# Performance work log

Hardware: AMD Instinct MI355X
Metric: run time of the kernel (lower is better)

The kernel has to match this reference:

```python
import jax, jax.numpy as jnp
import numpy as np

EPS = 1e-5
CONV_THRESHOLD = 0.0


def setup_inputs() -> dict:
    key = jax.random.key(0)
    ks = jax.random.split(key, 16)
    B, F = 65536, 256
    H1, H2 = 1024, 512
    d_in = F + 1  # raw features + 1 scalar conv feature
    inp = {
        "x": jax.random.normal(ks[0], (B, F), dtype=jnp.float32),
        # layer 1: Linear(d_in, H1) + BatchNorm1d(H1)
        "W1": jax.random.normal(ks[1], (d_in, H1), dtype=jnp.float32) * (1.0 / np.sqrt(d_in)),
        "b1": jax.random.normal(ks[2], (H1,), dtype=jnp.float32) * 0.01,
        "g1": jnp.ones((H1,), jnp.float32) + 0.1 * jax.random.normal(ks[3], (H1,), dtype=jnp.float32),
        "be1": jax.random.normal(ks[4], (H1,), dtype=jnp.float32) * 0.01,
        "m1": jax.random.normal(ks[5], (H1,), dtype=jnp.float32) * 0.1,
        "v1": jax.random.uniform(ks[6], (H1,), dtype=jnp.float32, minval=0.5, maxval=1.5),
        # layer 2: Linear(H1, H2) + BatchNorm1d(H2)
        "W2": jax.random.normal(ks[7], (H1, H2), dtype=jnp.float32) * (1.0 / np.sqrt(H1)),
        "b2": jax.random.normal(ks[8], (H2,), dtype=jnp.float32) * 0.01,
        "g2": jnp.ones((H2,), jnp.float32) + 0.1 * jax.random.normal(ks[9], (H2,), dtype=jnp.float32),
        "be2": jax.random.normal(ks[10], (H2,), dtype=jnp.float32) * 0.01,
        "m2": jax.random.normal(ks[11], (H2,), dtype=jnp.float32) * 0.1,
        "v2": jax.random.uniform(ks[12], (H2,), dtype=jnp.float32, minval=0.5, maxval=1.5),
        # output head: Linear(H2, 1)
        "W3": jax.random.normal(ks[13], (H2, 1), dtype=jnp.float32) * (1.0 / np.sqrt(H2)),
        "b3": jax.random.normal(ks[14], (1,), dtype=jnp.float32) * 0.01,
    }
    return inp


def _bn(h, g, be, m, v):
    # eval-mode BatchNorm1d with running statistics
    return g * (h - m) * jax.lax.rsqrt(v + EPS) + be


def reference(x, W1, b1, g1, be1, m1, v1, W2, b2, g2, be2, m2, v2, W3, b3):
    # Batched replacement of the per-sample numpy threshold conv:
    # the Conv filter reduces the whole sample patch with a mean and thresholds it,
    # producing one binary scalar feature per sample.  [B, 1]
    conv_feat = jnp.where(jnp.mean(x, axis=1, keepdims=True) > CONV_THRESHOLD, 1.0, 0.0).astype(x.dtype)
    h = jnp.concatenate([x, conv_feat], axis=1)  # [B, F+1]
    h = jax.nn.relu(_bn(h @ W1 + b1, g1, be1, m1, v1))  # [B, H1]
    h = jax.nn.relu(_bn(h @ W2 + b2, g2, be2, m2, v2))  # [B, H2]
    return jax.nn.sigmoid(h @ W3 + b3)  # [B, 1]
```

## Files before the change

kernel.cpp:

```cpp
#include <hip/hip_runtime.h>
#include <hip/hip_bf16.h>
#include <cstdint>
#include <cstddef>

typedef __bf16 bf16_t;
typedef bf16_t bf16x8 __attribute__((ext_vector_type(8)));
typedef float f32x4 __attribute__((ext_vector_type(4)));

#define BN_EPS 1e-5f

__device__ __forceinline__ void async_load16(const bf16_t* g, bf16_t* lds) {
  __builtin_amdgcn_global_load_lds(
      (__attribute__((address_space(1))) uint32_t*)(g),
      (__attribute__((address_space(3))) uint32_t*)(lds),
      16, 0, 0);
}

__global__ void prep_weights_kernel(const float* __restrict__ W1, const float* __restrict__ W2,
                                    const float* b1, const float* g1, const float* be1,
                                    const float* m1, const float* v1,
                                    const float* b2, const float* g2, const float* be2,
                                    const float* m2, const float* v2,
                                    bf16_t* __restrict__ W1T, bf16_t* __restrict__ W2T,
                                    float* s1, float* t1, float* s2, float* t2,
                                    float* w1last) {
  const int b = blockIdx.x;
  if (b < 192) {
    const float* src;
    bf16_t* dst;
    int R, C, bx, by;
    if (b < 64) { src = W1; dst = W1T; R = 256; C = 1024; bx = b & 15; by = b >> 4; }
    else        { src = W2; dst = W2T; R = 1024; C = 512; bx = (b - 64) & 7; by = (b - 64) >> 3; }
    __shared__ bf16_t tile[64][66];
    const int r0 = by * 64, c0 = bx * 64;
    const int tc = threadIdx.x & 63;
    const int tr4 = threadIdx.x >> 6;
#pragma unroll
    for (int i = 0; i < 16; ++i) {
      int r = i * 4 + tr4;
      tile[r][tc] = (bf16_t)src[(size_t)(r0 + r) * C + c0 + tc];
    }
    __syncthreads();
#pragma unroll
    for (int i = 0; i < 16; ++i) {
      int rr = i * 4 + tr4;
      dst[(size_t)(c0 + rr) * R + r0 + tc] = tile[tc][rr];
    }
  } else {
    for (int i = threadIdx.x; i < 1024; i += 256) {
      float s = g1[i] * rsqrtf(v1[i] + BN_EPS);
      s1[i] = s;
      t1[i] = be1[i] - m1[i] * s + b1[i] * s;
      w1last[i] = W1[256 * 1024 + i];
      if (i < 512) {
        float s2v = g2[i] * rsqrtf(v2[i] + BN_EPS);
        s2[i] = s2v;
        t2[i] = be2[i] - m2[i] * s2v + b2[i] * s2v;
      }
    }
  }
}

__global__ __launch_bounds__(256, 2) void fused_mlp(
    const float* __restrict__ x,
    const bf16_t* __restrict__ W1T, const bf16_t* __restrict__ W2T,
    const float* __restrict__ s1, const float* __restrict__ t1,
    const float* __restrict__ w1last,
    const float* __restrict__ s2, const float* __restrict__ t2,
    const float* __restrict__ W3, const float* __restrict__ b3,
    float* __restrict__ out) {
  __shared__ __align__(16) unsigned char smem[73728];
  const int tid = threadIdx.x;
  const int lane = tid & 63;
  const int w = tid >> 6;
  const int l15 = lane & 15;
  const int quad = lane >> 4;
  const int mTile = blockIdx.x * 64;

  bf16_t* As = (bf16_t*)smem;
  bf16_t* h1c = (bf16_t*)(smem + 32768);
  float* convs = (float*)(smem + 32768);
  bf16_t* B1s = (bf16_t*)(smem + 65536);
  float* outW = (float*)(smem + 65536);

  {
    const int rsub = lane >> 5;
    const int cc = lane & 31;
#pragma unroll
    for (int i = 0; i < 8; ++i) {
      int row = w * 16 + i * 2 + rsub;
      const float* gx = x + (size_t)(mTile + row) * 256 + cc * 8;
      const float4 a = *(const float4*)gx;
      const float4 bq = *(const float4*)(gx + 4);
      float s = a.x + a.y + a.z + a.w + bq.x + bq.y + bq.z + bq.w;
      bf16x8 v = {(bf16_t)a.x, (bf16_t)a.y, (bf16_t)a.z, (bf16_t)a.w,
                  (bf16_t)bq.x, (bf16_t)bq.y, (bf16_t)bq.z, (bf16_t)bq.w};
      *(bf16x8*)(As + row * 256 + (cc ^ (row & 7)) * 8) = v;
#pragma unroll
      for (int m = 1; m <= 16; m <<= 1) s += __shfl_xor(s, m);
      if (cc == 0) convs[row] = (s > 0.0f) ? 1.0f : 0.0f;
    }
  }
  __syncthreads();

  unsigned cmask = 0;
#pragma unroll
  for (int ti = 0; ti < 4; ++ti)
#pragma unroll
    for (int r = 0; r < 4; ++r)
      if (convs[ti * 16 + quad * 4 + r] > 0.5f) cmask |= (1u << (ti * 4 + r));

  bf16_t* B1w = B1s + w * 1024;
  const int srow = lane >> 2;
  const int schunk = (lane & 3) ^ ((lane >> 3) & 3);
  const int rchunk = quad ^ ((l15 >> 1) & 3);

  f32x4 acc2[4][8];
#pragma unroll
  for (int i = 0; i < 4; ++i)
#pragma unroll
    for (int j = 0; j < 8; ++j) {
      f32x4 z = {0.f, 0.f, 0.f, 0.f};
      acc2[i][j] = z;
    }

  for (int c = 0; c < 4; ++c) {
#pragma unroll
    for (int h = 0; h < 2; ++h) {
      const int colbase = c * 256 + w * 64 + h * 32;
      f32x4 acc1[4][2];
#pragma unroll
      for (int i = 0; i < 4; ++i)
#pragma unroll
        for (int t = 0; t < 2; ++t) {
          f32x4 z = {0.f, 0.f, 0.f, 0.f};
          acc1[i][t] = z;
        }

      const bf16_t* gB1 = W1T + (size_t)(colbase + srow) * 256 + schunk * 8;

#pragma unroll
      for (int i = 0; i < 2; ++i)
        async_load16(gB1 + (size_t)(i * 16) * 256, B1w + i * 512 + lane * 8);

      for (int ks = 0; ks < 8; ++ks) {
        asm volatile("s_waitcnt vmcnt(0)" ::: "memory");

        bf16x8 af[4], bfr[2];
#pragma unroll
        for (int tj = 0; tj < 2; ++tj)
          bfr[tj] = *(const bf16x8*)(B1w + (tj * 16 + l15) * 32 + rchunk * 8);
#pragma unroll
        for (int ti = 0; ti < 4; ++ti)
          af[ti] = *(const bf16x8*)(As + (ti * 16 + l15) * 256 +
                                    ((ks * 4 + quad) ^ (l15 & 7)) * 8);

        asm volatile("s_waitcnt lgkmcnt(0)" ::: "memory");
        if (ks < 7) {
#pragma unroll
          for (int i = 0; i < 2; ++i)
            async_load16(gB1 + (size_t)(i * 16) * 256 + (ks + 1) * 32,
                         B1w + i * 512 + lane * 8);
        }

#pragma unroll
        for (int ti = 0; ti < 4; ++ti)
#pragma unroll
          for (int tj = 0; tj < 2; ++tj)
            acc1[ti][tj] = __builtin_amdgcn_mfma_f32_16x16x32_bf16(af[ti], bfr[tj], acc1[ti][tj], 0, 0, 0);
      }

      if (h == 0) __syncthreads();

      float sc1[2], tc1[2], wl1[2];
#pragma unroll
      for (int tj = 0; tj < 2; ++tj) {
        int ccol = colbase + tj * 16 + l15;
        sc1[tj] = s1[ccol];
        tc1[tj] = t1[ccol];
        wl1[tj] = w1last[ccol];
      }
#pragma unroll
      for (int ti = 0; ti < 4; ++ti)
#pragma unroll
        for (int r = 0; r < 4; ++r) {
          const int rowl = ti * 16 + quad * 4 + r;
          const float cfv = ((cmask >> (ti * 4 + r)) & 1u) ? 1.0f : 0.0f;
#pragma unroll
          for (int tj = 0; tj < 2; ++tj) {
            float z = acc1[ti][tj][r] + cfv * wl1[tj];
            z = fmaxf(z * sc1[tj] + tc1[tj], 0.f);
            const int colc = w * 64 + h * 32 + tj * 16 + l15;
            const int c8 = (colc >> 3) ^ (rowl & 7);
            h1c[rowl * 256 + c8 * 8 + (l15 & 7)] = (bf16_t)z;
          }
        }
    }
    __syncthreads();

    const bf16_t* gB2 = W2T + (size_t)(w * 128 + l15) * 1024 + c * 256 + quad * 8;
#pragma unroll
    for (int s = 0; s < 8; ++s) {
      bf16x8 af2[4], bfr2[8];
#pragma unroll
      for (int tj = 0; tj < 8; ++tj)
        bfr2[tj] = *(const bf16x8*)(gB2 + (size_t)(tj * 16) * 1024 + s * 32);
#pragma unroll
      for (int ti = 0; ti < 4; ++ti)
        af2[ti] = *(const bf16x8*)(h1c + (ti * 16 + l15) * 256 +
                                   ((s * 4 + quad) ^ (l15 & 7)) * 8);
      __builtin_amdgcn_s_setprio(1);
#pragma unroll
      for (int ti = 0; ti < 4; ++ti)
#pragma unroll
        for (int tj = 0; tj < 8; ++tj)
          acc2[ti][tj] = __builtin_amdgcn_mfma_f32_16x16x32_bf16(af2[ti], bfr2[tj], acc2[ti][tj], 0, 0, 0);
      __builtin_amdgcn_s_setprio(0);
    }
  }

  float sc[8], tcs[8], w3c[8];
#pragma unroll
  for (int tj = 0; tj < 8; ++tj) {
    int ccol = w * 128 + tj * 16 + l15;
    sc[tj] = s2[ccol];
    tcs[tj] = t2[ccol];
    w3c[tj] = W3[ccol];
  }
  __syncthreads();
  float rowpv[4][4];
#pragma unroll
  for (int ti = 0; ti < 4; ++ti)
#pragma unroll
    for (int r = 0; r < 4; ++r) {
      float pv = 0.f;
#pragma unroll
      for (int tj = 0; tj < 8; ++tj) {
        float z = fmaxf(acc2[ti][tj][r] * sc[tj] + tcs[tj], 0.f);
        pv += z * w3c[tj];
      }
#pragma unroll
      for (int m = 1; m <= 8; m <<= 1) pv += __shfl_xor(pv, m);
      rowpv[ti][r] = pv;
    }
  if (l15 == 0) {
#pragma unroll
    for (int ti = 0; ti < 4; ++ti)
#pragma unroll
      for (int r = 0; r < 4; ++r)
        outW[w * 64 + ti * 16 + quad * 4 + r] = rowpv[ti][r];
  }
  __syncthreads();
  if (tid < 64) {
    float z = outW[tid] + outW[64 + tid] + outW[128 + tid] + outW[192 + tid] + b3[0];
    out[mTile + tid] = 1.0f / (1.0f + expf(-z));
  }
}

extern "C" void kernel_launch(void* const* d_in, const int* in_sizes, int n_in,
                              void* d_out, int out_size, void* d_ws, size_t ws_size,
                              hipStream_t stream) {
  const float* x = (const float*)d_in[0];
  const float* W1 = (const float*)d_in[1];
  const float* b1 = (const float*)d_in[2];
  const float* g1 = (const float*)d_in[3];
  const float* be1 = (const float*)d_in[4];
  const float* m1 = (const float*)d_in[5];
  const float* v1 = (const float*)d_in[6];
  const float* W2 = (const float*)d_in[7];
  const float* b2 = (const float*)d_in[8];
  const float* g2 = (const float*)d_in[9];
  const float* be2 = (const float*)d_in[10];
  const float* m2 = (const float*)d_in[11];
  const float* v2 = (const float*)d_in[12];
  const float* W3 = (const float*)d_in[13];
  const float* b3 = (const float*)d_in[14];
  float* out = (float*)d_out;

  char* p = (char*)d_ws;
  bf16_t* h1 = (bf16_t*)p;       p += (size_t)65536 * 1024 * 2;
  float* partials = (float*)p;   p += (size_t)4 * 65536 * 4;
  bf16_t* W1T = (bf16_t*)p;      p += (size_t)1024 * 256 * 2;
  bf16_t* W2T = (bf16_t*)p;      p += (size_t)512 * 1024 * 2;
  float* w1last = (float*)p;     p += 1024 * 4;
  float* s1 = (float*)p;         p += 1024 * 4;
  float* t1 = (float*)p;         p += 1024 * 4;
  float* s2 = (float*)p;         p += 512 * 4;
  float* t2 = (float*)p;         p += 512 * 4;
  (void)h1;
  (void)partials;

  prep_weights_kernel<<<193, 256, 0, stream>>>(W1, W2, b1, g1, be1, m1, v1,
                                               b2, g2, be2, m2, v2,
                                               W1T, W2T, s1, t1, s2, t2, w1last);

  fused_mlp<<<1024, 256, 0, stream>>>(x, W1T, W2T, s1, t1, w1last,
                                      s2, t2, W3, b3, out);
}
```

Baseline: 308.6 us.

## Split fused MLP block across eight waves and double-buffer W1 tile loads

Doubles the block to 512 threads so each wave owns half as many layer-1 and layer-2 output columns, and raises the launch-bounds occupancy target. The layer-1 weight staging becomes a two-slot LDS ring with vmcnt(1) waits so the next K-slice load overlaps the MFMAs. LDS grows to hold per-wave buffers for eight waves and the final reduction sums eight partials. The tighter register budget implied by the launch bounds may cause spills of the accumulators.

```diff
diff --git a/kernel.cpp b/kernel.cpp
--- a/kernel.cpp
+++ b/kernel.cpp
@@ -61,7 +61,7 @@
   }
 }
 
-__global__ __launch_bounds__(256, 2) void fused_mlp(
+__global__ __launch_bounds__(512, 4) void fused_mlp(
     const float* __restrict__ x,
     const bf16_t* __restrict__ W1T, const bf16_t* __restrict__ W2T,
     const float* __restrict__ s1, const float* __restrict__ t1,
@@ -69,7 +69,7 @@
     const float* __restrict__ s2, const float* __restrict__ t2,
     const float* __restrict__ W3, const float* __restrict__ b3,
     float* __restrict__ out) {
-  __shared__ __align__(16) unsigned char smem[73728];
+  __shared__ __align__(16) unsigned char smem[81920];
   const int tid = threadIdx.x;
   const int lane = tid & 63;
   const int w = tid >> 6;
@@ -87,8 +87,8 @@
     const int rsub = lane >> 5;
     const int cc = lane & 31;
 #pragma unroll
-    for (int i = 0; i < 8; ++i) {
-      int row = w * 16 + i * 2 + rsub;
+    for (int i = 0; i < 4; ++i) {
+      int row = w * 8 + i * 2 + rsub;
       const float* gx = x + (size_t)(mTile + row) * 256 + cc * 8;
       const float4 a = *(const float4*)gx;
       const float4 bq = *(const float4*)(gx + 4);
@@ -109,101 +109,91 @@
 #pragma unroll
     for (int r = 0; r < 4; ++r)
       if (convs[ti * 16 + quad * 4 + r] > 0.5f) cmask |= (1u << (ti * 4 + r));
+  __syncthreads();
 
   bf16_t* B1w = B1s + w * 1024;
   const int srow = lane >> 2;
   const int schunk = (lane & 3) ^ ((lane >> 3) & 3);
   const int rchunk = quad ^ ((l15 >> 1) & 3);
 
-  f32x4 acc2[4][8];
+  f32x4 acc2[4][4];
 #pragma unroll
   for (int i = 0; i < 4; ++i)
 #pragma unroll
-    for (int j = 0; j < 8; ++j) {
+    for (int j = 0; j < 4; ++j) {
       f32x4 z = {0.f, 0.f, 0.f, 0.f};
       acc2[i][j] = z;
     }
 
   for (int c = 0; c < 4; ++c) {
 #pragma unroll
-    for (int h = 0; h < 2; ++h) {
-      const int colbase = c * 256 + w * 64 + h * 32;
-      f32x4 acc1[4][2];
-#pragma unroll
-      for (int i = 0; i < 4; ++i)
-#pragma unroll
-        for (int t = 0; t < 2; ++t) {
-          f32x4 z = {0.f, 0.f, 0.f, 0.f};
-          acc1[i][t] = z;
-        }
+    for (int sp = 0; sp < 2; ++sp) {
+      const int colbase = c * 256 + w * 32 + sp * 16;
+      f32x4 acc1[4];
+#pragma unroll
+      for (int i = 0; i < 4; ++i) {
+        f32x4 z = {0.f, 0.f, 0.f, 0.f};
+        acc1[i] = z;
+      }
 
       const bf16_t* gB1 = W1T + (size_t)(colbase + srow) * 256 + schunk * 8;
 
-#pragma unroll
-      for (int i = 0; i < 2; ++i)
-        async_load16(gB1 + (size_t)(i * 16) * 256, B1w + i * 512 + lane * 8);
+      async_load16(gB1, B1w + lane * 8);
+      async_load16(gB1 + 32, B1w + 512 + lane * 8);
 
       for (int ks = 0; ks < 8; ++ks) {
-        asm volatile("s_waitcnt vmcnt(0)" ::: "memory");
-
-        bf16x8 af[4], bfr[2];
-#pragma unroll
-        for (int tj = 0; tj < 2; ++tj)
-          bfr[tj] = *(const bf16x8*)(B1w + (tj * 16 + l15) * 32 + rchunk * 8);
+        if (ks < 7)
+          asm volatile("s_waitcnt vmcnt(1)" ::: "memory");
+        else
+          asm volatile("s_waitcnt vmcnt(0)" ::: "memory");
+        __builtin_amdgcn_sched_barrier(0);
+
+        bf16x8 bfr = *(const bf16x8*)(B1w + (ks & 1) * 512 + l15 * 32 + rchunk * 8);
+        bf16x8 af[4];
 #pragma unroll
         for (int ti = 0; ti < 4; ++ti)
           af[ti] = *(const bf16x8*)(As + (ti * 16 + l15) * 256 +
                                     ((ks * 4 + quad) ^ (l15 & 7)) * 8);
 
         asm volatile("s_waitcnt lgkmcnt(0)" ::: "memory");
-        if (ks < 7) {
-#pragma unroll
-          for (int i = 0; i < 2; ++i)
-            async_load16(gB1 + (size_t)(i * 16) * 256 + (ks + 1) * 32,
-                         B1w + i * 512 + lane * 8);
-        }
-
+        __builtin_amdgcn_sched_barrier(0);
+        if (ks < 6)
+          async_load16(gB1 + (ks + 2) * 32, B1w + (ks & 1) * 512 + lane * 8);
+
+        __builtin_amdgcn_s_setprio(1);
 #pragma unroll
         for (int ti = 0; ti < 4; ++ti)
-#pragma unroll
-          for (int tj = 0; tj < 2; ++tj)
-            acc1[ti][tj] = __builtin_amdgcn_mfma_f32_16x16x32_bf16(af[ti], bfr[tj], acc1[ti][tj], 0, 0, 0);
-      }
-
-      if (h == 0) __syncthreads();
-
-      float sc1[2], tc1[2], wl1[2];
-#pragma unroll
-      for (int tj = 0; tj < 2; ++tj) {
-        int ccol = colbase + tj * 16 + l15;
-        sc1[tj] = s1[ccol];
-        tc1[tj] = t1[ccol];
-        wl1[tj] = w1last[ccol];
-      }
+          acc1[ti] = __builtin_amdgcn_mfma_f32_16x16x32_bf16(af[ti], bfr, acc1[ti], 0, 0, 0);
+        __builtin_amdgcn_s_setprio(0);
+      }
+
+      if (sp == 0) __syncthreads();
+
+      const int ccol = colbase + l15;
+      const float sc1 = s1[ccol];
+      const float tc1 = t1[ccol];
+      const float wl1 = w1last[ccol];
+      const int colc = w * 32 + sp * 16 + l15;
 #pragma unroll
       for (int ti = 0; ti < 4; ++ti)
 #pragma unroll
         for (int r = 0; r < 4; ++r) {
           const int rowl = ti * 16 + quad * 4 + r;
           const float cfv = ((cmask >> (ti * 4 + r)) & 1u) ? 1.0f : 0.0f;
-#pragma unroll
-          for (int tj = 0; tj < 2; ++tj) {
-            float z = acc1[ti][tj][r] + cfv * wl1[tj];
-            z = fmaxf(z * sc1[tj] + tc1[tj], 0.f);
-            const int colc = w * 64 + h * 32 + tj * 16 + l15;
-            const int c8 = (colc >> 3) ^ (rowl & 7);
-            h1c[rowl * 256 + c8 * 8 + (l15 & 7)] = (bf16_t)z;
-          }
+          float z = acc1[ti][r] + cfv * wl1;
+          z = fmaxf(z * sc1 + tc1, 0.f);
+          const int c8 = (colc >> 3) ^ (rowl & 7);
+          h1c[rowl * 256 + c8 * 8 + (l15 & 7)] = (bf16_t)z;
         }
     }
     __syncthreads();
 
-    const bf16_t* gB2 = W2T + (size_t)(w * 128 + l15) * 1024 + c * 256 + quad * 8;
+    const bf16_t* gB2 = W2T + (size_t)(w * 64 + l15) * 1024 + c * 256 + quad * 8;
 #pragma unroll
     for (int s = 0; s < 8; ++s) {
-      bf16x8 af2[4], bfr2[8];
-#pragma unroll
-      for (int tj = 0; tj < 8; ++tj)
+      bf16x8 af2[4], bfr2[4];
+#pragma unroll
+      for (int tj = 0; tj < 4; ++tj)
         bfr2[tj] = *(const bf16x8*)(gB2 + (size_t)(tj * 16) * 1024 + s * 32);
 #pragma unroll
       for (int ti = 0; ti < 4; ++ti)
@@ -213,21 +203,20 @@
 #pragma unroll
       for (int ti = 0; ti < 4; ++ti)
 #pragma unroll
-        for (int tj = 0; tj < 8; ++tj)
+        for (int tj = 0; tj < 4; ++tj)
           acc2[ti][tj] = __builtin_amdgcn_mfma_f32_16x16x32_bf16(af2[ti], bfr2[tj], acc2[ti][tj], 0, 0, 0);
       __builtin_amdgcn_s_setprio(0);
     }
   }
 
-  float sc[8], tcs[8], w3c[8];
-#pragma unroll
-  for (int tj = 0; tj < 8; ++tj) {
-    int ccol = w * 128 + tj * 16 + l15;
+  float sc[4], tcs[4], w3c[4];
+#pragma unroll
+  for (int tj = 0; tj < 4; ++tj) {
+    int ccol = w * 64 + tj * 16 + l15;
     sc[tj] = s2[ccol];
     tcs[tj] = t2[ccol];
     w3c[tj] = W3[ccol];
   }
-  __syncthreads();
   float rowpv[4][4];
 #pragma unroll
   for (int ti = 0; ti < 4; ++ti)
@@ -235,7 +224,7 @@
     for (int r = 0; r < 4; ++r) {
       float pv = 0.f;
 #pragma unroll
-      for (int tj = 0; tj < 8; ++tj) {
+      for (int tj = 0; tj < 4; ++tj) {
         float z = fmaxf(acc2[ti][tj][r] * sc[tj] + tcs[tj], 0.f);
         pv += z * w3c[tj];
       }
@@ -252,7 +241,9 @@
   }
   __syncthreads();
   if (tid < 64) {
-    float z = outW[tid] + outW[64 + tid] + outW[128 + tid] + outW[192 + tid] + b3[0];
+    float z = b3[0];
+#pragma unroll
+    for (int k = 0; k < 8; ++k) z += outW[k * 64 + tid];
     out[mTile + tid] = 1.0f / (1.0f + expf(-z));
   }
 }
@@ -294,6 +285,6 @@
                                                b2, g2, be2, m2, v2,
                                                W1T, W2T, s1, t1, s2, t2, w1last);
 
-  fused_mlp<<<1024, 256, 0, stream>>>(x, W1T, W2T, s1, t1, w1last,
+  fused_mlp<<<1024, 512, 0, stream>>>(x, W1T, W2T, s1, t1, w1last,
                                       s2, t2, W3, b3, out);
 }
```

Result: slower. 363.6 us (+17.8%).
